# Kernel tuning notes

Measured on AMD Instinct MI355X. Metric: run time of the kernel, lower is better.

Reference implementation:

```python
import jax, jax.numpy as jnp
import numpy as np

H = 12       # num attention heads
D = 64       # head dim
K = 6        # heads activated: max(1, int(H * top_k_percent)), top_k_percent=0.5
EPS = 1e-12  # BERT LayerNorm eps


def setup_inputs() -> dict:
    key = jax.random.key(0)
    ks = jax.random.split(key, 8)
    hid = H * D
    sc = 0.02
    return {
        'hidden_states': jax.random.normal(ks[0], (8, 1024, hid), jnp.float32),
        'Wq': jax.random.normal(ks[1], (hid, hid), jnp.float32) * sc,
        'bq': jnp.zeros((hid,), jnp.float32),
        'Wk': jax.random.normal(ks[2], (hid, hid), jnp.float32) * sc,
        'bk': jnp.zeros((hid,), jnp.float32),
        'Wv': jax.random.normal(ks[3], (hid, hid), jnp.float32) * sc,
        'bv': jnp.zeros((hid,), jnp.float32),
        'Wr': jax.random.normal(ks[4], (hid, H), jnp.float32) * sc,
        'br': jnp.zeros((H,), jnp.float32),
        'Wo': jax.random.normal(ks[5], (hid, hid), jnp.float32) * sc,
        'bo': jnp.zeros((hid,), jnp.float32),
        'ln_g': jnp.ones((hid,), jnp.float32),
        'ln_b': jnp.zeros((hid,), jnp.float32),
    }


def reference(hidden_states, Wq, bq, Wk, bk, Wv, bv, Wr, br, Wo, bo, ln_g, ln_b):
    B, S, hid = hidden_states.shape
    # Router: mean-pooled tokens -> per-head logits -> straight-through top-k mask
    router_in = hidden_states.mean(axis=1)                      # [B, hid]
    logits = router_in @ Wr + br                                # [B, H]
    _, top_idx = jax.lax.top_k(logits, K)                       # [B, K]
    hard = jax.nn.one_hot(top_idx, H, dtype=logits.dtype).sum(axis=1)  # [B, H]
    head_mask = hard + logits - jax.lax.stop_gradient(logits)   # straight-through
    m = head_mask[:, :, None, None]                             # [B, H, 1, 1]

    def proj(W, b):
        return (hidden_states @ W + b).reshape(B, S, H, D).transpose(0, 2, 1, 3)

    q = proj(Wq, bq) * m
    k = proj(Wk, bk) * m
    v = proj(Wv, bv) * m

    scores = jnp.einsum('bhqd,bhkd->bhqk', q, k) / jnp.sqrt(jnp.float32(D))
    probs = jax.nn.softmax(scores, axis=-1)
    ctx = jnp.einsum('bhqk,bhkd->bhqd', probs, v)               # [B, H, S, D]
    ctx = ctx.transpose(0, 2, 1, 3).reshape(B, S, hid)

    # BertSelfOutput: dense -> (dropout=identity in eval) -> residual -> LayerNorm
    x = ctx @ Wo + bo + hidden_states
    mu = x.mean(axis=-1, keepdims=True)
    var = ((x - mu) ** 2).mean(axis=-1, keepdims=True)
    return ((x - mu) / jnp.sqrt(var + EPS)) * ln_g + ln_b
```

## Files before the change

### kernel.cpp

```cpp
#include <hip/hip_runtime.h>

typedef __bf16 bf16;
typedef __bf16 bf16x2_t __attribute__((ext_vector_type(2)));
typedef __bf16 bf16x4_t __attribute__((ext_vector_type(4)));
typedef __bf16 bf16x8 __attribute__((ext_vector_type(8)));
typedef float  f32x4  __attribute__((ext_vector_type(4)));

__device__ __forceinline__ void async16(const void* g, void* l) {
  __builtin_amdgcn_global_load_lds(
      (__attribute__((address_space(1))) void*)(g),
      (__attribute__((address_space(3))) void*)(l), 16, 0, 0);
}

__device__ __forceinline__ f32x4 mfma16(bf16x8 a, bf16x8 b, f32x4 c) {
  return __builtin_amdgcn_mfma_f32_16x16x32_bf16(a, b, c, 0, 0, 0);
}

__global__ __launch_bounds__(256) void prep_k(
    const float* __restrict__ hs, bf16* __restrict__ hsb, float* __restrict__ partial,
    const float* __restrict__ s0, const float* __restrict__ s1,
    const float* __restrict__ s2, const float* __restrict__ s3,
    bf16* __restrict__ d0, bf16* __restrict__ d1,
    bf16* __restrict__ d2, bf16* __restrict__ d3) {
  __shared__ bf16 tile[32][33];
  int id = blockIdx.x;
  int t = threadIdx.x;
  if (id < 2304) {
    int z = id / 576, rem = id % 576;
    int by = rem / 24, bx = rem % 24;
    const float* in = (z == 0) ? s0 : (z == 1) ? s1 : (z == 2) ? s2 : s3;
    bf16* out       = (z == 0) ? d0 : (z == 1) ? d1 : (z == 2) ? d2 : d3;
    int c0 = bx * 32, r0 = by * 32;
#pragma unroll
    for (int i = 0; i < 4; ++i) {
      int idx = t + i * 256;
      int r = idx >> 5, c = idx & 31;
      tile[r][c] = (bf16)in[(size_t)(r0 + r) * 768 + (c0 + c)];
    }
    __syncthreads();
#pragma unroll
    for (int i = 0; i < 4; ++i) {
      int idx = t + i * 256;
      int r = idx >> 5, c = idx & 31;
      out[(size_t)(c0 + r) * 768 + (r0 + c)] = tile[c][r];
    }
  } else {
    int id2 = id - 2304;
    int b = id2 & 7, g = id2 >> 3;
    if (t >= 192) return;
    const float* p = hs  + ((size_t)b * 1024 + g * 32) * 768 + t * 4;
    bf16*        q = hsb + ((size_t)b * 1024 + g * 32) * 768 + t * 4;
    float4 a = {0.f, 0.f, 0.f, 0.f};
    for (int s = 0; s < 32; ++s) {
      float4 v = *(const float4*)(p + (size_t)s * 768);
      a.x += v.x; a.y += v.y; a.z += v.z; a.w += v.w;
      bf16x4_t o;
      o[0] = (bf16)v.x; o[1] = (bf16)v.y; o[2] = (bf16)v.z; o[3] = (bf16)v.w;
      *(bf16x4_t*)(q + (size_t)s * 768) = o;
    }
    *(float4*)(partial + ((size_t)b * 32 + g) * 768 + t * 4) = a;
  }
}

__global__ __launch_bounds__(256) void router_final_k(const float* __restrict__ Wr,
                                                      const float* __restrict__ br,
                                                      const float* __restrict__ partial,
                                                      float* __restrict__ mask,
                                                      int* __restrict__ actH) {
  int b = blockIdx.x, t = threadIdx.x;
  int w = t >> 6;
  __shared__ float mean_s[768];
  __shared__ float red[4][12];
  __shared__ float lg[12];
  for (int c = t; c < 768; c += 256) {
    float a = 0.f;
    for (int g = 0; g < 32; ++g) a += partial[((size_t)b * 32 + g) * 768 + c];
    mean_s[c] = a * (1.0f / 1024.0f);
  }
  __syncthreads();
  float a[12];
#pragma unroll
  for (int h = 0; h < 12; ++h) a[h] = 0.f;
#pragma unroll
  for (int j = 0; j < 3; ++j) {
    int c = t + j * 256;
    float m = mean_s[c];
    const float* wr = Wr + c * 12;
#pragma unroll
    for (int h = 0; h < 12; ++h) a[h] += m * wr[h];
  }
#pragma unroll
  for (int off = 1; off < 64; off <<= 1)
#pragma unroll
    for (int h = 0; h < 12; ++h) a[h] += __shfl_xor(a[h], off);
  if ((t & 63) == 0)
#pragma unroll
    for (int h = 0; h < 12; ++h) red[w][h] = a[h];
  __syncthreads();
  if (t == 0) {
#pragma unroll
    for (int h = 0; h < 12; ++h)
      lg[h] = br[h] + red[0][h] + red[1][h] + red[2][h] + red[3][h];
    unsigned chosen = 0;
    for (int j = 0; j < 6; ++j) {
      int bi = -1; float bv = -1e30f;
      for (int h = 0; h < 12; ++h)
        if (!((chosen >> h) & 1) && lg[h] > bv) { bv = lg[h]; bi = h; }
      chosen |= 1u << bi;
    }
    int k = 0;
    for (int h = 0; h < 12; ++h) {
      mask[b * 12 + h] = ((chosen >> h) & 1) ? 1.f : 0.f;
      if ((chosen >> h) & 1) actH[b * 6 + (k++)] = h;
    }
  }
}

__global__ __launch_bounds__(256, 3) void gemm_qkv_k(
    const bf16* __restrict__ X, const bf16* __restrict__ Wcat,
    const float* __restrict__ bq, const float* __restrict__ bk, const float* __restrict__ bv,
    const int* __restrict__ actH,
    bf16* __restrict__ Qo, bf16* __restrict__ Ko, bf16* __restrict__ Vto) {
  __shared__ __align__(16) bf16 Al[128 * 64];
  __shared__ __align__(16) bf16 Bl[128 * 64];
  int mt64 = blockIdx.x;
  int sp   = blockIdx.y;
  int z    = blockIdx.z;
  int b    = mt64 >> 3;
  int h0   = actH[b * 6 + sp * 2];
  int h1   = actH[b * 6 + sp * 2 + 1];
  int m0   = mt64 * 128;

  const float* bia = (z == 0) ? bq : (z == 1) ? bk : bv;
  int t = threadIdx.x, w = t >> 6, lane = t & 63, lrow = lane & 15, quad = lane >> 4;
  int wm = (w >> 1) * 64, wn = (w & 1) * 64;

  int srow = t >> 3;
  int sch  = (t & 7) ^ (srow & 7);
  const bf16* aptr[4];
  const bf16* bptr[4];
#pragma unroll
  for (int i = 0; i < 4; ++i) {
    aptr[i] = X + (size_t)(m0 + i * 32 + srow) * 768 + sch * 8;
    int hh = (i < 2) ? h0 : h1;
    int rr = (i & 1) * 32 + srow;
    bptr[i] = Wcat + (size_t)(z * 768 + hh * 64 + rr) * 768 + sch * 8;
  }

  int ra_base = wm + lrow, rb_base = wn + lrow;
  const bf16* baA[2];
  const bf16* baB[2];
#pragma unroll
  for (int ks = 0; ks < 2; ++ks) {
    baA[ks] = &Al[ra_base * 64 + (((ks * 4 + quad) ^ (ra_base & 7)) * 8)];
    baB[ks] = &Bl[rb_base * 64 + (((ks * 4 + quad) ^ (rb_base & 7)) * 8)];
  }

  f32x4 acc[4][4];
#pragma unroll
  for (int a = 0; a < 4; ++a)
#pragma unroll
    for (int c = 0; c < 4; ++c) acc[a][c] = (f32x4){0.f, 0.f, 0.f, 0.f};

  for (int k0 = 0; k0 < 768; k0 += 64) {
#pragma unroll
    for (int i = 0; i < 4; ++i) {
      async16(aptr[i], &Al[(i * 256 + t) * 8]);
      aptr[i] += 64;
    }
#pragma unroll
    for (int i = 0; i < 4; ++i) {
      async16(bptr[i], &Bl[(i * 256 + t) * 8]);
      bptr[i] += 64;
    }
    __syncthreads();
    bf16x8 af[2][4], bfr[2][4];
#pragma unroll
    for (int ks = 0; ks < 2; ++ks)
#pragma unroll
      for (int i = 0; i < 4; ++i) {
        af[ks][i]  = *(const bf16x8*)(baA[ks] + i * 1024);
        bfr[ks][i] = *(const bf16x8*)(baB[ks] + i * 1024);
      }
#pragma unroll
    for (int ks = 0; ks < 2; ++ks)
#pragma unroll
      for (int mt = 0; mt < 4; ++mt)
#pragma unroll
        for (int nt2 = 0; nt2 < 4; ++nt2)
          acc[mt][nt2] = mfma16(af[ks][mt], bfr[ks][nt2], acc[mt][nt2]);
    __syncthreads();
  }

  float biasv[4];
#pragma unroll
  for (int nt2 = 0; nt2 < 4; ++nt2) {
    int nl = wn + nt2 * 16 + lrow;
    int hh = (nl >> 6) ? h1 : h0;
    biasv[nt2] = bia[hh * 64 + (nl & 63)];
  }

  if (z == 2) {
#pragma unroll
    for (int mt = 0; mt < 4; ++mt)
#pragma unroll
      for (int nt2 = 0; nt2 < 4; ++nt2) {
        int s = (m0 + wm + mt * 16 + quad * 4) & 1023;
        int nl = wn + nt2 * 16 + lrow;
        int hh = (nl >> 6) ? h1 : h0;
        int d = nl & 63;
        bf16x4_t pk;
#pragma unroll
        for (int r = 0; r < 4; ++r) pk[r] = (bf16)(acc[mt][nt2][r] + biasv[nt2]);
        *(bf16x4_t*)&Vto[(((size_t)b * 12 + hh) * 64 + d) * 1024 + s] = pk;
      }
  } else {
    bf16* Out = (z == 0) ? Qo : Ko;
#pragma unroll
    for (int mt = 0; mt < 4; ++mt)
#pragma unroll
      for (int nt2 = 0; nt2 < 4; ++nt2)
#pragma unroll
        for (int r = 0; r < 4; ++r) {
          int s = (m0 + wm + mt * 16 + quad * 4 + r) & 1023;
          int nl = wn + nt2 * 16 + lrow;
          int hh = (nl >> 6) ? h1 : h0;
          int d = nl & 63;
          Out[(((size_t)b * 12 + hh) * 1024 + s) * 64 + d] =
              (bf16)(acc[mt][nt2][r] + biasv[nt2]);
        }
  }
}

__global__ __launch_bounds__(256, 3) void attn_k(
    const bf16* __restrict__ Q, const bf16* __restrict__ K, const bf16* __restrict__ Vt,
    const int* __restrict__ actH, bf16* __restrict__ ctx) {
  int ai = blockIdx.x, qt = blockIdx.y;
  int bb = ai / 6, slot = ai - bb * 6;
  int h = actH[bb * 6 + slot];
  int bh = bb * 12 + h;
  int t = threadIdx.x, w = t >> 6, lane = t & 63, lrow = lane & 15, quad = lane >> 4;

  __shared__ __align__(16) bf16 K_lds[128 * 64];
  __shared__ __align__(16) bf16 V_lds[64 * 128];
  __shared__ __align__(16) bf16 P_lds[4][16 * 136];

  const bf16* Qh = Q  + (size_t)bh * 65536;
  const bf16* Kh = K  + (size_t)bh * 65536;
  const bf16* Vh = Vt + (size_t)bh * 65536;

  bf16x8 qf[2][2];
#pragma unroll
  for (int mt = 0; mt < 2; ++mt)
#pragma unroll
    for (int ks = 0; ks < 2; ++ks)
      qf[mt][ks] = *(const bf16x8*)&Qh[(size_t)(qt * 128 + w * 32 + mt * 16 + lrow) * 64 + ks * 32 + quad * 8];

  f32x4 o_acc[2][4];
  float m_i[2][4], l_i[2][4];
#pragma unroll
  for (int mt = 0; mt < 2; ++mt) {
#pragma unroll
    for (int dt = 0; dt < 4; ++dt) o_acc[mt][dt] = (f32x4){0.f, 0.f, 0.f, 0.f};
#pragma unroll
    for (int r = 0; r < 4; ++r) { m_i[mt][r] = -INFINITY; l_i[mt][r] = 0.f; }
  }

  for (int kt = 0; kt < 8; ++kt) {
#pragma unroll
    for (int i = 0; i < 4; ++i) {
      int c = i * 256 + t;
      int r = c >> 3, ch = (c & 7) ^ (r & 7);
      async16(Kh + (size_t)kt * 8192 + r * 64 + ch * 8, &K_lds[c * 8]);
    }
#pragma unroll
    for (int i = 0; i < 4; ++i) {
      int c = i * 256 + t;
      int r = c >> 4, ch = (c & 15) ^ (r & 7);
      async16(Vh + (size_t)r * 1024 + kt * 128 + ch * 8, &V_lds[c * 8]);
    }
    __syncthreads();

#pragma unroll
    for (int mt = 0; mt < 2; ++mt) {
      f32x4 s_acc[8];
#pragma unroll
      for (int nt = 0; nt < 8; ++nt) s_acc[nt] = (f32x4){0.f, 0.f, 0.f, 0.f};
      __builtin_amdgcn_s_setprio(1);
#pragma unroll
      for (int nt = 0; nt < 8; ++nt) {
        int rb = nt * 16 + lrow;
#pragma unroll
        for (int ks = 0; ks < 2; ++ks) {
          bf16x8 kf = *(const bf16x8*)&K_lds[rb * 64 + (((ks * 4 + quad) ^ (rb & 7)) * 8)];
          s_acc[nt] = mfma16(qf[mt][ks], kf, s_acc[nt]);
        }
      }
      __builtin_amdgcn_s_setprio(0);
#pragma unroll
      for (int nt = 0; nt < 8; ++nt) s_acc[nt] = s_acc[nt] * 0.125f;

      float mx[4];
#pragma unroll
      for (int r = 0; r < 4; ++r) {
        float m = s_acc[0][r];
#pragma unroll
        for (int nt = 1; nt < 8; ++nt) m = fmaxf(m, s_acc[nt][r]);
        m = fmaxf(m, __shfl_xor(m, 1));
        m = fmaxf(m, __shfl_xor(m, 2));
        m = fmaxf(m, __shfl_xor(m, 4));
        m = fmaxf(m, __shfl_xor(m, 8));
        mx[r] = m;
      }
      bool grow = false;
#pragma unroll
      for (int r = 0; r < 4; ++r) grow = grow || (mx[r] > m_i[mt][r] + 8.f);
      if (__any(grow)) {
#pragma unroll
        for (int r = 0; r < 4; ++r) {
          float mold = m_i[mt][r];
          float mnew = fmaxf(mold, mx[r]);
          float alpha = __expf(mold - mnew);
          m_i[mt][r] = mnew;
          l_i[mt][r] *= alpha;
#pragma unroll
          for (int dt = 0; dt < 4; ++dt) o_acc[mt][dt][r] *= alpha;
        }
      }
#pragma unroll
      for (int r = 0; r < 4; ++r) {
        float mnew = m_i[mt][r];
        float rs = 0.f;
#pragma unroll
        for (int nt = 0; nt < 8; ++nt) {
          float pv = __expf(s_acc[nt][r] - mnew);
          rs += pv;
          P_lds[w][(quad * 4 + r) * 136 + nt * 16 + lrow] = (bf16)pv;
        }
        rs += __shfl_xor(rs, 1);
        rs += __shfl_xor(rs, 2);
        rs += __shfl_xor(rs, 4);
        rs += __shfl_xor(rs, 8);
        l_i[mt][r] += rs;
      }

      bf16x8 pf[4];
#pragma unroll
      for (int ks = 0; ks < 4; ++ks)
        pf[ks] = *(const bf16x8*)&P_lds[w][lrow * 136 + ks * 32 + quad * 8];
      __builtin_amdgcn_s_setprio(1);
#pragma unroll
      for (int dt = 0; dt < 4; ++dt) {
        int rv = dt * 16 + lrow;
#pragma unroll
        for (int ks = 0; ks < 4; ++ks) {
          bf16x8 vf = *(const bf16x8*)&V_lds[rv * 128 + (((ks * 4 + quad) ^ (rv & 7)) * 8)];
          o_acc[mt][dt] = mfma16(pf[ks], vf, o_acc[mt][dt]);
        }
      }
      __builtin_amdgcn_s_setprio(0);
    }
    __syncthreads();
  }

#pragma unroll
  for (int mt = 0; mt < 2; ++mt)
#pragma unroll
    for (int r = 0; r < 4; ++r) {
      float inv = 1.0f / l_i[mt][r];
      int s = qt * 128 + w * 32 + mt * 16 + quad * 4 + r;
#pragma unroll
      for (int dt = 0; dt < 4; ++dt) {
        int d = dt * 16 + lrow;
        ctx[((size_t)(bb * 1024 + s)) * 768 + h * 64 + d] = (bf16)(o_acc[mt][dt][r] * inv);
      }
    }
}

__global__ __launch_bounds__(256, 3) void gemm_out_k(
    const bf16* __restrict__ Cx, const bf16* __restrict__ Wot,
    const float* __restrict__ bo, const float* __restrict__ res,
    const float* __restrict__ mask,
    float* __restrict__ xo) {
  __shared__ __align__(16) bf16 Al[128 * 64];
  __shared__ __align__(16) bf16 Bl[128 * 64];
  int bid = blockIdx.x;
  int xcd = bid & 7, idx = bid >> 3;
  int nt = idx % 6, mt8 = idx / 6;
  int m0 = (mt8 * 8 + xcd) * 128;
  int n0 = nt * 128;
  int t = threadIdx.x, w = t >> 6, lane = t & 63, lrow = lane & 15, quad = lane >> 4;
  int wm = (w >> 1) * 64, wn = (w & 1) * 64;

  int bb = m0 >> 10;
  unsigned am = 0;
#pragma unroll
  for (int hh = 0; hh < 12; ++hh)
    am |= (mask[bb * 12 + hh] != 0.f) ? (1u << hh) : 0u;

  int srow = t >> 3;
  int sch  = (t & 7) ^ (srow & 7);
  const bf16* aptr[4];
  const bf16* bptr[4];
#pragma unroll
  for (int i = 0; i < 4; ++i) {
    aptr[i] = Cx  + (size_t)(m0 + i * 32 + srow) * 768 + sch * 8;
    bptr[i] = Wot + (size_t)(n0 + i * 32 + srow) * 768 + sch * 8;
  }
  int ra_base = wm + lrow, rb_base = wn + lrow;
  const bf16* baA[2];
  const bf16* baB[2];
#pragma unroll
  for (int ks = 0; ks < 2; ++ks) {
    baA[ks] = &Al[ra_base * 64 + (((ks * 4 + quad) ^ (ra_base & 7)) * 8)];
    baB[ks] = &Bl[rb_base * 64 + (((ks * 4 + quad) ^ (rb_base & 7)) * 8)];
  }

  f32x4 acc[4][4];
#pragma unroll
  for (int a = 0; a < 4; ++a)
#pragma unroll
    for (int b = 0; b < 4; ++b) acc[a][b] = (f32x4){0.f, 0.f, 0.f, 0.f};

  for (int k0 = 0; k0 < 768; k0 += 64) {
    if (am & (1u << (k0 >> 6))) {
#pragma unroll
      for (int i = 0; i < 4; ++i) async16(aptr[i], &Al[(i * 256 + t) * 8]);
#pragma unroll
      for (int i = 0; i < 4; ++i) async16(bptr[i], &Bl[(i * 256 + t) * 8]);
      __syncthreads();
      bf16x8 af[2][4], bfr[2][4];
#pragma unroll
      for (int ks = 0; ks < 2; ++ks)
#pragma unroll
        for (int i = 0; i < 4; ++i) {
          af[ks][i]  = *(const bf16x8*)(baA[ks] + i * 1024);
          bfr[ks][i] = *(const bf16x8*)(baB[ks] + i * 1024);
        }
#pragma unroll
      for (int ks = 0; ks < 2; ++ks)
#pragma unroll
        for (int mt = 0; mt < 4; ++mt)
#pragma unroll
          for (int nt2 = 0; nt2 < 4; ++nt2)
            acc[mt][nt2] = mfma16(af[ks][mt], bfr[ks][nt2], acc[mt][nt2]);
      __syncthreads();
    }
#pragma unroll
    for (int i = 0; i < 4; ++i) { aptr[i] += 64; bptr[i] += 64; }
  }

  float biasv[4];
#pragma unroll
  for (int nt2 = 0; nt2 < 4; ++nt2) biasv[nt2] = bo[n0 + wn + nt2 * 16 + lrow];

#pragma unroll
  for (int mt = 0; mt < 4; ++mt)
#pragma unroll
    for (int nt2 = 0; nt2 < 4; ++nt2)
#pragma unroll
      for (int r = 0; r < 4; ++r) {
        int m = m0 + wm + mt * 16 + quad * 4 + r;
        int n = n0 + wn + nt2 * 16 + lrow;
        xo[(size_t)m * 768 + n] = acc[mt][nt2][r] + biasv[nt2] + res[(size_t)m * 768 + n];
      }
}

__global__ __launch_bounds__(256) void ln_k(const float* __restrict__ x,
                                            const float* __restrict__ g,
                                            const float* __restrict__ be,
                                            float* __restrict__ out) {
  int row = blockIdx.x, t = threadIdx.x;
  const float* xr = x + (size_t)row * 768;
  float v0 = xr[t], v1 = xr[t + 256], v2 = xr[t + 512];
  float s = v0 + v1 + v2;
  float s2 = v0 * v0 + v1 * v1 + v2 * v2;
#pragma unroll
  for (int off = 32; off > 0; off >>= 1) {
    s  += __shfl_down(s, off);
    s2 += __shfl_down(s2, off);
  }
  __shared__ float red[8];
  if ((t & 63) == 0) { red[(t >> 6) * 2] = s; red[(t >> 6) * 2 + 1] = s2; }
  __syncthreads();
  if (t == 0) {
    float a = 0.f, b2 = 0.f;
    for (int i = 0; i < 4; ++i) { a += red[2 * i]; b2 += red[2 * i + 1]; }
    float mu = a * (1.0f / 768.0f);
    float var = b2 * (1.0f / 768.0f) - mu * mu;
    red[0] = mu;
    red[1] = rsqrtf(var + 1e-12f);
  }
  __syncthreads();
  float mu = red[0], rs = red[1];
  out[(size_t)row * 768 + t]       = (v0 - mu) * rs * g[t]       + be[t];
  out[(size_t)row * 768 + t + 256] = (v1 - mu) * rs * g[t + 256] + be[t + 256];
  out[(size_t)row * 768 + t + 512] = (v2 - mu) * rs * g[t + 512] + be[t + 512];
}

extern "C" void kernel_launch(void* const* d_in, const int* in_sizes, int n_in,
                              void* d_out, int out_size, void* d_ws, size_t ws_size,
                              hipStream_t stream) {
  const float* hs  = (const float*)d_in[0];
  const float* Wq  = (const float*)d_in[1];
  const float* bq  = (const float*)d_in[2];
  const float* Wk  = (const float*)d_in[3];
  const float* bk  = (const float*)d_in[4];
  const float* Wv  = (const float*)d_in[5];
  const float* bv  = (const float*)d_in[6];
  const float* Wr  = (const float*)d_in[7];
  const float* br  = (const float*)d_in[8];
  const float* Wo  = (const float*)d_in[9];
  const float* bo  = (const float*)d_in[10];
  const float* lng = (const float*)d_in[11];
  const float* lnb = (const float*)d_in[12];
  float* out = (float*)d_out;
  dim3 blk(256);

  char* p = (char*)d_ws;
  float* maskp = (float*)p; p += 512;
  int*   actI  = (int*)p;   p += 256;
  float* partial = (float*)p; p += (size_t)8 * 32 * 768 * 4;
  bf16* hsb  = (bf16*)p; p += (size_t)8192 * 768 * 2;
  bf16* Wcat = (bf16*)p; p += (size_t)2304 * 768 * 2;
  bf16* Wot  = (bf16*)p; p += (size_t)768 * 768 * 2;

  prep_k<<<dim3(2560), blk, 0, stream>>>(hs, hsb, partial,
      Wq, Wk, Wv, Wo, Wcat, Wcat + 768 * 768, Wcat + 1536 * 768, Wot);
  router_final_k<<<dim3(8), blk, 0, stream>>>(Wr, br, partial, maskp, actI);

  size_t used_common = (size_t)(p - (char*)d_ws);
  size_t need_big = used_common + 3 * (size_t)8192 * 768 * 2;

  if (ws_size >= need_big) {
    char* qk_base = p;
    bf16* Qb  = (bf16*)p; p += (size_t)8192 * 768 * 2;
    bf16* Kb  = (bf16*)p; p += (size_t)8192 * 768 * 2;
    bf16* Vtb = (bf16*)p;
    float* Xb = (float*)qk_base;
    bf16* Ctx = (bf16*)d_out;

    gemm_qkv_k<<<dim3(64, 3, 3), blk, 0, stream>>>(hsb, Wcat, bq, bk, bv, actI, Qb, Kb, Vtb);
    attn_k<<<dim3(48, 8), blk, 0, stream>>>(Qb, Kb, Vtb, actI, Ctx);
    gemm_out_k<<<dim3(8 * 8 * 6), blk, 0, stream>>>(Ctx, Wot, bo, hs, maskp, Xb);
    ln_k<<<dim3(8192), blk, 0, stream>>>(Xb, lng, lnb, out);
  } else {
    bf16* Qb  = (bf16*)p; p += (size_t)1024 * 768 * 2;
    bf16* Kb  = (bf16*)p; p += (size_t)1024 * 768 * 2;
    bf16* Vtb = (bf16*)p; p += (size_t)1024 * 768 * 2;
    bf16* Ctx = (bf16*)p; p += (size_t)1024 * 768 * 2;
    float* Xb = (float*)p; p += (size_t)1024 * 768 * 4;

    for (int b = 0; b < 8; ++b) {
      const bf16* hsb_b = hsb + (size_t)b * 1024 * 768;
      const float* hs_b = hs + (size_t)b * 1024 * 768;
      float* outb = out + (size_t)b * 1024 * 768;
      gemm_qkv_k<<<dim3(8, 3, 3), blk, 0, stream>>>(hsb_b, Wcat, bq, bk, bv, actI + b * 6, Qb, Kb, Vtb);
      attn_k<<<dim3(6, 8), blk, 0, stream>>>(Qb, Kb, Vtb, actI + b * 6, Ctx);
      gemm_out_k<<<dim3(8 * 1 * 6), blk, 0, stream>>>(Ctx, Wot, bo, hs_b, maskp + b * 12, Xb);
      ln_k<<<dim3(1024), blk, 0, stream>>>(Xb, lng, lnb, outb);
    }
  }
}
```

Before: 208.3 us.

## Fuse router into prep and LayerNorm into output GEMM via last-block counters

Removes the separate router launch: the last prep block to finish for each batch (found with an atomic counter) computes the router mean, logits and top-k mask. It also removes the separate LayerNorm launch: the last of the six N-tile blocks for each 128-row M tile normalises those rows straight from the freshly written x buffer. Ctx now lives in the hsb buffer instead of the output buffer, since the output is now written inside the GEMM kernel. This cuts two kernel launches and their gaps, at the cost of a memset, atomics and threadfences, and of a serialized LN tail that runs on only a few blocks.

```diff
diff --git a/kernel.cpp b/kernel.cpp
--- a/kernel.cpp
+++ b/kernel.cpp
@@ -21,8 +21,14 @@
     const float* __restrict__ s0, const float* __restrict__ s1,
     const float* __restrict__ s2, const float* __restrict__ s3,
     bf16* __restrict__ d0, bf16* __restrict__ d1,
-    bf16* __restrict__ d2, bf16* __restrict__ d3) {
+    bf16* __restrict__ d2, bf16* __restrict__ d3,
+    const float* __restrict__ Wr, const float* __restrict__ br,
+    int* __restrict__ rcnt, float* __restrict__ mask, int* __restrict__ actH) {
   __shared__ bf16 tile[32][33];
+  __shared__ float mean_s[768];
+  __shared__ float red[4][12];
+  __shared__ float lg[12];
+  __shared__ int lastf;
   int id = blockIdx.x;
   int t = threadIdx.x;
   if (id < 2304) {
@@ -44,10 +50,11 @@
       int r = idx >> 5, c = idx & 31;
       out[(size_t)(c0 + r) * 768 + (r0 + c)] = tile[c][r];
     }
-  } else {
-    int id2 = id - 2304;
-    int b = id2 & 7, g = id2 >> 3;
-    if (t >= 192) return;
+    return;
+  }
+  int id2 = id - 2304;
+  int b = id2 & 7, g = id2 >> 3;
+  if (t < 192) {
     const float* p = hs  + ((size_t)b * 1024 + g * 32) * 768 + t * 4;
     bf16*        q = hsb + ((size_t)b * 1024 + g * 32) * 768 + t * 4;
     float4 a = {0.f, 0.f, 0.f, 0.f};
@@ -60,24 +67,19 @@
     }
     *(float4*)(partial + ((size_t)b * 32 + g) * 768 + t * 4) = a;
   }
-}
-
-__global__ __launch_bounds__(256) void router_final_k(const float* __restrict__ Wr,
-                                                      const float* __restrict__ br,
-                                                      const float* __restrict__ partial,
-                                                      float* __restrict__ mask,
-                                                      int* __restrict__ actH) {
-  int b = blockIdx.x, t = threadIdx.x;
-  int w = t >> 6;
-  __shared__ float mean_s[768];
-  __shared__ float red[4][12];
-  __shared__ float lg[12];
+  __threadfence();
+  __syncthreads();
+  if (t == 0) lastf = (atomicAdd(&rcnt[b], 1) == 31) ? 1 : 0;
+  __syncthreads();
+  if (lastf == 0) return;
+  __threadfence();
   for (int c = t; c < 768; c += 256) {
     float a = 0.f;
-    for (int g = 0; g < 32; ++g) a += partial[((size_t)b * 32 + g) * 768 + c];
+    for (int gg = 0; gg < 32; ++gg) a += partial[((size_t)b * 32 + gg) * 768 + c];
     mean_s[c] = a * (1.0f / 1024.0f);
   }
   __syncthreads();
+  int w = t >> 6;
   float a[12];
 #pragma unroll
   for (int h = 0; h < 12; ++h) a[h] = 0.f;
@@ -381,9 +383,12 @@
     const bf16* __restrict__ Cx, const bf16* __restrict__ Wot,
     const float* __restrict__ bo, const float* __restrict__ res,
     const float* __restrict__ mask,
-    float* __restrict__ xo) {
+    float* __restrict__ xo,
+    int* __restrict__ gcnt, const float* __restrict__ lng,
+    const float* __restrict__ lnb, float* __restrict__ outp) {
   __shared__ __align__(16) bf16 Al[128 * 64];
   __shared__ __align__(16) bf16 Bl[128 * 64];
+  __shared__ int lastf;
   int bid = blockIdx.x;
   int xcd = bid & 7, idx = bid >> 3;
   int nt = idx % 6, mt8 = idx / 6;
@@ -464,6 +469,49 @@
         int n = n0 + wn + nt2 * 16 + lrow;
         xo[(size_t)m * 768 + n] = acc[mt][nt2][r] + biasv[nt2] + res[(size_t)m * 768 + n];
       }
+
+  if (!gcnt) return;
+  __threadfence();
+  __syncthreads();
+  if (t == 0) lastf = (atomicAdd(&gcnt[mt8 * 8 + xcd], 1) == 5) ? 1 : 0;
+  __syncthreads();
+  if (lastf == 0) return;
+  __threadfence();
+  const float4* g4 = (const float4*)lng;
+  const float4* b4 = (const float4*)lnb;
+  for (int i = 0; i < 32; ++i) {
+    int row = m0 + w * 32 + i;
+    const float4* xr4 = (const float4*)(xo + (size_t)row * 768);
+    float4 xv0 = xr4[lane], xv1 = xr4[lane + 64], xv2 = xr4[lane + 128];
+    float s  = xv0.x + xv0.y + xv0.z + xv0.w
+             + xv1.x + xv1.y + xv1.z + xv1.w
+             + xv2.x + xv2.y + xv2.z + xv2.w;
+    float s2 = xv0.x*xv0.x + xv0.y*xv0.y + xv0.z*xv0.z + xv0.w*xv0.w
+             + xv1.x*xv1.x + xv1.y*xv1.y + xv1.z*xv1.z + xv1.w*xv1.w
+             + xv2.x*xv2.x + xv2.y*xv2.y + xv2.z*xv2.z + xv2.w*xv2.w;
+#pragma unroll
+    for (int off = 32; off > 0; off >>= 1) {
+      s  += __shfl_xor(s, off);
+      s2 += __shfl_xor(s2, off);
+    }
+    float mu = s * (1.0f / 768.0f);
+    float var = s2 * (1.0f / 768.0f) - mu * mu;
+    float rsq = rsqrtf(var + 1e-12f);
+    float4* or4 = (float4*)(outp + (size_t)row * 768);
+    float4 gv, bv, o;
+    gv = g4[lane];       bv = b4[lane];
+    o.x = (xv0.x - mu) * rsq * gv.x + bv.x; o.y = (xv0.y - mu) * rsq * gv.y + bv.y;
+    o.z = (xv0.z - mu) * rsq * gv.z + bv.z; o.w = (xv0.w - mu) * rsq * gv.w + bv.w;
+    or4[lane] = o;
+    gv = g4[lane + 64];  bv = b4[lane + 64];
+    o.x = (xv1.x - mu) * rsq * gv.x + bv.x; o.y = (xv1.y - mu) * rsq * gv.y + bv.y;
+    o.z = (xv1.z - mu) * rsq * gv.z + bv.z; o.w = (xv1.w - mu) * rsq * gv.w + bv.w;
+    or4[lane + 64] = o;
+    gv = g4[lane + 128]; bv = b4[lane + 128];
+    o.x = (xv2.x - mu) * rsq * gv.x + bv.x; o.y = (xv2.y - mu) * rsq * gv.y + bv.y;
+    o.z = (xv2.z - mu) * rsq * gv.z + bv.z; o.w = (xv2.w - mu) * rsq * gv.w + bv.w;
+    or4[lane + 128] = o;
+  }
 }
 
 __global__ __launch_bounds__(256) void ln_k(const float* __restrict__ x,
@@ -520,14 +568,18 @@
   char* p = (char*)d_ws;
   float* maskp = (float*)p; p += 512;
   int*   actI  = (int*)p;   p += 256;
+  int*   rcnt  = (int*)p;   p += 64;
+  int*   gcnt  = (int*)p;   p += 256;
   float* partial = (float*)p; p += (size_t)8 * 32 * 768 * 4;
   bf16* hsb  = (bf16*)p; p += (size_t)8192 * 768 * 2;
   bf16* Wcat = (bf16*)p; p += (size_t)2304 * 768 * 2;
   bf16* Wot  = (bf16*)p; p += (size_t)768 * 768 * 2;
 
+  hipMemsetAsync(rcnt, 0, 320, stream);
+
   prep_k<<<dim3(2560), blk, 0, stream>>>(hs, hsb, partial,
-      Wq, Wk, Wv, Wo, Wcat, Wcat + 768 * 768, Wcat + 1536 * 768, Wot);
-  router_final_k<<<dim3(8), blk, 0, stream>>>(Wr, br, partial, maskp, actI);
+      Wq, Wk, Wv, Wo, Wcat, Wcat + 768 * 768, Wcat + 1536 * 768, Wot,
+      Wr, br, rcnt, maskp, actI);
 
   size_t used_common = (size_t)(p - (char*)d_ws);
   size_t need_big = used_common + 3 * (size_t)8192 * 768 * 2;
@@ -538,12 +590,12 @@
     bf16* Kb  = (bf16*)p; p += (size_t)8192 * 768 * 2;
     bf16* Vtb = (bf16*)p;
     float* Xb = (float*)qk_base;
-    bf16* Ctx = (bf16*)d_out;
+    bf16* Ctx = hsb;
 
     gemm_qkv_k<<<dim3(64, 3, 3), blk, 0, stream>>>(hsb, Wcat, bq, bk, bv, actI, Qb, Kb, Vtb);
     attn_k<<<dim3(48, 8), blk, 0, stream>>>(Qb, Kb, Vtb, actI, Ctx);
-    gemm_out_k<<<dim3(8 * 8 * 6), blk, 0, stream>>>(Ctx, Wot, bo, hs, maskp, Xb);
-    ln_k<<<dim3(8192), blk, 0, stream>>>(Xb, lng, lnb, out);
+    gemm_out_k<<<dim3(8 * 8 * 6), blk, 0, stream>>>(Ctx, Wot, bo, hs, maskp, Xb,
+                                                    gcnt, lng, lnb, out);
   } else {
     bf16* Qb  = (bf16*)p; p += (size_t)1024 * 768 * 2;
     bf16* Kb  = (bf16*)p; p += (size_t)1024 * 768 * 2;
@@ -557,7 +609,8 @@
       float* outb = out + (size_t)b * 1024 * 768;
       gemm_qkv_k<<<dim3(8, 3, 3), blk, 0, stream>>>(hsb_b, Wcat, bq, bk, bv, actI + b * 6, Qb, Kb, Vtb);
       attn_k<<<dim3(6, 8), blk, 0, stream>>>(Qb, Kb, Vtb, actI + b * 6, Ctx);
-      gemm_out_k<<<dim3(8 * 1 * 6), blk, 0, stream>>>(Ctx, Wot, bo, hs_b, maskp + b * 12, Xb);
+      gemm_out_k<<<dim3(8 * 1 * 6), blk, 0, stream>>>(Ctx, Wot, bo, hs_b, maskp + b * 12, Xb,
+                                                      (int*)nullptr, lng, lnb, outb);
       ln_k<<<dim3(1024), blk, 0, stream>>>(Xb, lng, lnb, outb);
     }
   }
```

Result: slower. 330.8 us (+58.9%).
